# Kernel tuning notes

Hardware: AMD Instinct MI355X
Metric: run time of the kernel (lower is better)

The kernel has to match this reference:

```python
import jax, jax.numpy as jnp
import numpy as np

N_MODES = 512
LOOP_LENGTHS = [1]  # tbi.loop_lengths (single loop of delay 1)


def _bs_schedule(n_modes, loop_lengths):
    """Static application schedule, matching the torch loop order.

    Returns (theta index k, mode i, delay d) for each step, in the order the
    rotations are right-multiplied into the unitary: U = ((I @ R_{K-1}) @ ...) @ R_0.
    """
    K = sum(n_modes - d for d in loop_lengths)
    ks, iis, dds = [], [], []
    ci = K - 1
    for delay in reversed(loop_lengths):
        for i in reversed(range(n_modes - delay)):
            ks.append(ci)
            iis.append(i)
            dds.append(delay)
            ci -= 1
    return np.array(ks), np.array(iis), np.array(dds)


def setup_inputs() -> dict:
    key = jax.random.key(0)
    K = sum(N_MODES - d for d in LOOP_LENGTHS)  # 511 beam splitters
    thetas = jax.random.normal(key, (K,), dtype=jnp.float32)
    return {"thetas": thetas}


def reference(thetas):
    ks, iis, dds = _bs_schedule(N_MODES, LOOP_LENGTHS)
    # cos/sin gathered into application order
    c = jnp.cos(thetas)[ks]
    s = jnp.sin(thetas)[ks]
    ia = jnp.asarray(iis, dtype=jnp.int32)           # first mode of each rotation
    ib = jnp.asarray(iis + dds, dtype=jnp.int32)     # second mode (i + delay)

    U0 = jnp.eye(N_MODES, dtype=thetas.dtype)

    def step(U, xs):
        ck, sk, a, b = xs
        # Right-multiply by Givens rotation R with R[a,a]=c, R[a,b]=s, R[b,a]=-s, R[b,b]=c
        col_a = U[:, a]
        col_b = U[:, b]
        U = U.at[:, a].set(ck * col_a - sk * col_b)
        U = U.at[:, b].set(sk * col_a + ck * col_b)
        return U, None

    U, _ = jax.lax.scan(step, U0, (c, s, ia, ib))
    return U
```

## Files before the change

### kernel.cpp

```cpp
#include <hip/hip_runtime.h>

#define NM  512
#define KTH 511

__global__ __launch_bounds__(64) void unitary_rows(const float* __restrict__ thetas,
                                                   float* __restrict__ U) {
    const int r    = blockIdx.x;
    const int lane = threadIdx.x;

    __shared__ float row[NM];

    #pragma unroll
    for (int k = 0; k < NM / 64; ++k) row[lane + 64 * k] = 0.0f;
    __syncthreads();

    const int   L  = r;
    const float cr = (r < KTH) ? cosf(thetas[r]) : 1.0f;

    float sv[8], cv[8];
    float p = 1.0f;
    #pragma unroll
    for (int mm = 0; mm < 8; ++mm) {
        const int m = lane * 8 + mm;
        if (m < L) {
            const int   i  = r - 1 - m;
            const float th = thetas[i];
            sv[mm] = sinf(th);
            cv[mm] = cosf(th);
            p *= -sv[mm];
        } else {
            sv[mm] = 0.0f;
            cv[mm] = 0.0f;
        }
    }

    float x = p;
    #pragma unroll
    for (int off = 1; off < 64; off <<= 1) {
        const float y = __shfl_up(x, off, 64);
        if (lane >= off) x *= y;
    }
    float pre = __shfl_up(x, 1, 64);
    if (lane == 0) pre = 1.0f;

    float Q = cr * pre;
    #pragma unroll
    for (int mm = 0; mm < 8; ++mm) {
        const int m = lane * 8 + mm;
        if (m < L) {
            const int i = r - 1 - m;
            row[i + 1] = cv[mm] * Q;
            Q          = -sv[mm] * Q;
            if (m == L - 1) row[0] = Q;
        }
    }
    if (r == 0 && lane == 0) row[0] = cr;
    if (r < KTH && lane == 0) row[r + 1] = sinf(thetas[r]);
    __syncthreads();

    float4*       dst = (float4*)(U + (size_t)r * NM);
    const float4* src = (const float4*)row;
    dst[lane]      = src[lane];
    dst[lane + 64] = src[lane + 64];
}

extern "C" void kernel_launch(void* const* d_in, const int* in_sizes, int n_in,
                              void* d_out, int out_size, void* d_ws, size_t ws_size,
                              hipStream_t stream) {
    const float* thetas = (const float*)d_in[0];
    float*       U      = (float*)d_out;
    unitary_rows<<<NM, 64, 0, stream>>>(thetas, U);
}
```

Before: 56.11 us.

## Batch eight rows per block and share a precomputed sin/cos table in LDS

Each block now handles eight rows with one wave per row. All 511 cos/sin values are computed once per block into padded shared-memory tables, instead of each row recomputing transcendentals from global thetas. The row buffer is no longer zero-initialised; zeros past the row's support are written by predicated selects in the store loop. Padding the index reduces LDS bank conflicts. The grid shrinks to 64 blocks, which lowers parallelism across CUs in exchange for less redundant sin/cos work.

```diff
diff --git a/kernel.cpp b/kernel.cpp
--- a/kernel.cpp
+++ b/kernel.cpp
@@ -1,21 +1,32 @@
 #include <hip/hip_runtime.h>
 
-#define NM  512
-#define KTH 511
+#define NM   512
+#define KTH  511
+#define ROWS 8
+#define NTHR (ROWS * 64)
+#define PADI(i) ((i) + ((i) >> 3))
+#define PLEN 576
 
-__global__ __launch_bounds__(64) void unitary_rows(const float* __restrict__ thetas,
-                                                   float* __restrict__ U) {
-    const int r    = blockIdx.x;
-    const int lane = threadIdx.x;
+__global__ __launch_bounds__(NTHR) void unitary_rows(const float* __restrict__ thetas,
+                                                     float* __restrict__ U) {
+    const int tid  = threadIdx.x;
+    const int lane = tid & 63;
+    const int w    = tid >> 6;
+    const int r    = blockIdx.x * ROWS + w;
 
-    __shared__ float row[NM];
+    __shared__ float c_tab[PLEN];
+    __shared__ float s_tab[PLEN];
+    __shared__ float rowpad[ROWS][PLEN];
 
-    #pragma unroll
-    for (int k = 0; k < NM / 64; ++k) row[lane + 64 * k] = 0.0f;
+    if (tid < KTH) {
+        const float th = thetas[tid];
+        c_tab[PADI(tid)] = cosf(th);
+        s_tab[PADI(tid)] = sinf(th);
+    }
     __syncthreads();
 
     const int   L  = r;
-    const float cr = (r < KTH) ? cosf(thetas[r]) : 1.0f;
+    const float cr = (r < KTH) ? c_tab[PADI(r)] : 1.0f;
 
     float sv[8], cv[8];
     float p = 1.0f;
@@ -23,10 +34,9 @@
     for (int mm = 0; mm < 8; ++mm) {
         const int m = lane * 8 + mm;
         if (m < L) {
-            const int   i  = r - 1 - m;
-            const float th = thetas[i];
-            sv[mm] = sinf(th);
-            cv[mm] = cosf(th);
+            const int i = r - 1 - m;
+            sv[mm] = s_tab[PADI(i)];
+            cv[mm] = c_tab[PADI(i)];
             p *= -sv[mm];
         } else {
             sv[mm] = 0.0f;
@@ -49,19 +59,27 @@
         const int m = lane * 8 + mm;
         if (m < L) {
             const int i = r - 1 - m;
-            row[i + 1] = cv[mm] * Q;
-            Q          = -sv[mm] * Q;
-            if (m == L - 1) row[0] = Q;
+            rowpad[w][PADI(i + 1)] = cv[mm] * Q;
+            Q = -sv[mm] * Q;
+            if (m == L - 1) rowpad[w][0] = Q;
         }
     }
-    if (r == 0 && lane == 0) row[0] = cr;
-    if (r < KTH && lane == 0) row[r + 1] = sinf(thetas[r]);
+    if (r == 0 && lane == 0)  rowpad[w][0] = cr;
+    if (r < KTH && lane == 0) rowpad[w][PADI(r + 1)] = s_tab[PADI(r)];
     __syncthreads();
 
-    float4*       dst = (float4*)(U + (size_t)r * NM);
-    const float4* src = (const float4*)row;
-    dst[lane]      = src[lane];
-    dst[lane + 64] = src[lane + 64];
+    float4* dst = (float4*)(U + (size_t)r * NM);
+    #pragma unroll
+    for (int t = 0; t < 2; ++t) {
+        const int j  = lane + 64 * t;
+        const int c0 = 4 * j;
+        float4 v;
+        v.x = (c0     <= r + 1) ? rowpad[w][PADI(c0)]     : 0.0f;
+        v.y = (c0 + 1 <= r + 1) ? rowpad[w][PADI(c0 + 1)] : 0.0f;
+        v.z = (c0 + 2 <= r + 1) ? rowpad[w][PADI(c0 + 2)] : 0.0f;
+        v.w = (c0 + 3 <= r + 1) ? rowpad[w][PADI(c0 + 3)] : 0.0f;
+        dst[j] = v;
+    }
 }
 
 extern "C" void kernel_launch(void* const* d_in, const int* in_sizes, int n_in,
@@ -69,5 +87,5 @@
                               hipStream_t stream) {
     const float* thetas = (const float*)d_in[0];
     float*       U      = (float*)d_out;
-    unitary_rows<<<NM, 64, 0, stream>>>(thetas, U);
+    unitary_rows<<<NM / ROWS, NTHR, 0, stream>>>(thetas, U);
 }
```

Measured after the change: 54.01 us. -3.7%, faster.
